# Optimization experiments

Measured on AMD Instinct MI355X. Metric: run time of the kernel, lower is better.

## Reference

```python
import jax, jax.numpy as jnp
import numpy as np

N = 50000
C = 128
E = 800000
STEPS = 3


def setup_inputs() -> dict:
    key = jax.random.key(0)
    ks = jax.random.split(key, 8)
    x = jax.random.normal(ks[0], (N, C), dtype=jnp.float32)
    edge_index = jax.random.randint(ks[1], (2, E), 0, N, dtype=jnp.int64)
    s = 1.0 / np.sqrt(C)
    W_lin = jax.random.uniform(ks[2], (C, C), jnp.float32, -s, s)   # nn.Linear(C, C, bias=False)
    W_ih = jax.random.uniform(ks[3], (3 * C, C), jnp.float32, -s, s)  # GRUCell weight_ih
    W_hh = jax.random.uniform(ks[4], (3 * C, C), jnp.float32, -s, s)  # GRUCell weight_hh
    b_ih = jax.random.uniform(ks[5], (3 * C,), jnp.float32, -s, s)
    b_hh = jax.random.uniform(ks[6], (3 * C,), jnp.float32, -s, s)
    return {"x": x, "edge_index": edge_index, "W_lin": W_lin,
            "W_ih": W_ih, "W_hh": W_hh, "b_ih": b_ih, "b_hh": b_hh}


def _gru_cell(inp, h, W_ih, W_hh, b_ih, b_hh):
    # torch.nn.GRUCell math
    gi = inp @ W_ih.T + b_ih   # [N, 3C]
    gh = h @ W_hh.T + b_hh     # [N, 3C]
    i_r, i_z, i_n = jnp.split(gi, 3, axis=-1)
    h_r, h_z, h_n = jnp.split(gh, 3, axis=-1)
    r = jax.nn.sigmoid(i_r + h_r)
    z = jax.nn.sigmoid(i_z + h_z)
    n = jnp.tanh(i_n + r * h_n)
    return (1.0 - z) * n + z * h


def reference(x, edge_index, W_lin, W_ih, W_hh, b_ih, b_hh):
    src = edge_index[0]
    dst = edge_index[1]
    state = x
    for _ in range(STEPS):
        m = state @ W_lin.T                       # [N, C] dense transform
        msgs = jnp.take(m, src, axis=0)           # [E, C] gather
        propagated = jax.ops.segment_sum(msgs, dst, num_segments=N)  # scatter-add
        state = _gru_cell(propagated, state, W_ih, W_hh, b_ih, b_hh)
    return state
```

## Files before the change

### kernel.cpp

```cpp
#include <hip/hip_runtime.h>

#define NN 50000
#define CC 128
#define EE 800000
#define NT 1563
#define NBLK 196

typedef short bf16x8 __attribute__((ext_vector_type(8)));
typedef float f32x4 __attribute__((ext_vector_type(4)));

__device__ __forceinline__ float bf2f(unsigned int u16) {
  union { unsigned int u; float f; } x; x.u = u16 << 16; return x.f;
}
__device__ __forceinline__ unsigned short f2bf(float f) {
  union { float f; unsigned int u; } x; x.f = f;
  unsigned int u = x.u;
  unsigned int r = (u + 0x7fffu + ((u >> 16) & 1u)) >> 16;
  return (unsigned short)r;
}

__global__ void cast_f2b_k(const float* __restrict__ in, unsigned short* __restrict__ out, int n4) {
  int i = blockIdx.x * blockDim.x + threadIdx.x;
  int stride = gridDim.x * blockDim.x;
  for (; i < n4; i += stride) {
    float4 v = ((const float4*)in)[i];
    ushort4 o;
    o.x = f2bf(v.x); o.y = f2bf(v.y); o.z = f2bf(v.z); o.w = f2bf(v.w);
    ((ushort4*)out)[i] = o;
  }
}

__global__ __launch_bounds__(256) void wcomp_k(const float* __restrict__ Wih,
                                               const float* __restrict__ Wlin,
                                               unsigned short* __restrict__ Wcb) {
  int gid = blockIdx.x * 256 + threadIdx.x;
  int i = gid >> 7, j = gid & 127;
  float acc = 0.f;
  #pragma unroll 8
  for (int k = 0; k < 128; ++k)
    acc += Wih[i * 128 + k] * Wlin[k * 128 + j];
  Wcb[i * 128 + j] = f2bf(acc);
}

__global__ void zero_k(int* __restrict__ p, int n) {
  int i = blockIdx.x * blockDim.x + threadIdx.x;
  if (i < n) p[i] = 0;
}

__global__ void hist_k(const int* __restrict__ dst, int* __restrict__ cnt, int n) {
  int i = blockIdx.x * blockDim.x + threadIdx.x;
  if (i < n) atomicAdd(&cnt[dst[i]], 1);
}

__global__ __launch_bounds__(256) void scan1_k(const int* __restrict__ cnt,
                                               int* __restrict__ rowptr,
                                               int* __restrict__ bsum, int N) {
  __shared__ int wtot[4];
  int tid = threadIdx.x, lane = tid & 63, w = tid >> 6;
  int i = blockIdx.x * 256 + tid;
  int v = (i < N) ? cnt[i] : 0;
  int x = v;
  #pragma unroll
  for (int off = 1; off < 64; off <<= 1) {
    int t = __shfl_up(x, off, 64);
    if (lane >= off) x += t;
  }
  if (lane == 63) wtot[w] = x;
  __syncthreads();
  int woff = 0;
  for (int j = 0; j < w; ++j) woff += wtot[j];
  int excl = x - v + woff;
  if (i < N) rowptr[i] = excl;
  if (tid == 255) bsum[blockIdx.x] = excl + v;
}

__global__ __launch_bounds__(256) void scan2_k(int* __restrict__ bsum, int* __restrict__ rowptr, int NB) {
  __shared__ int wtot[4];
  int tid = threadIdx.x, lane = tid & 63, w = tid >> 6;
  int v = (tid < NB) ? bsum[tid] : 0;
  int x = v;
  #pragma unroll
  for (int off = 1; off < 64; off <<= 1) {
    int t = __shfl_up(x, off, 64);
    if (lane >= off) x += t;
  }
  if (lane == 63) wtot[w] = x;
  __syncthreads();
  int woff = 0;
  for (int j = 0; j < w; ++j) woff += wtot[j];
  int excl = x - v + woff;
  if (tid < NB) bsum[tid] = excl;
  if (tid == 255) rowptr[NN] = excl + v;
}

__global__ void scan3_k(int* __restrict__ rowptr, const int* __restrict__ bsum,
                        int* __restrict__ cursor, int N) {
  int i = blockIdx.x * 256 + threadIdx.x;
  if (i < N) {
    int r = rowptr[i] + bsum[i >> 8];
    rowptr[i] = r;
    cursor[i] = r;
  }
}

__global__ void fill_k(const int* __restrict__ src, const int* __restrict__ dst,
                       int* __restrict__ cursor, int* __restrict__ colx, int n) {
  int i = blockIdx.x * blockDim.x + threadIdx.x;
  if (i < n) {
    int pos = atomicAdd(&cursor[dst[i]], 1);
    colx[pos] = src[i];
  }
}

__global__ __launch_bounds__(256) void agg2_k(const unsigned short* __restrict__ M,
                                              const int* __restrict__ rowptr,
                                              const int* __restrict__ colx,
                                              unsigned short* __restrict__ P, int N) {
  int wid = (blockIdx.x * 256 + threadIdx.x) >> 6;
  int lane = threadIdx.x & 63;
  if (wid >= N) return;
  int beg = rowptr[wid], end = rowptr[wid + 1];
  int half = lane >> 5, li = lane & 31;
  float a0 = 0.f, a1 = 0.f, a2 = 0.f, a3 = 0.f;
  int n = end - beg;
  int i = 0;
  for (; i + 8 <= n; i += 8) {
    int e = beg + i + half;
    int s0 = colx[e], s1 = colx[e + 2], s2 = colx[e + 4], s3 = colx[e + 6];
    uint2 v0 = *(const uint2*)(M + s0 * CC + li * 4);
    uint2 v1 = *(const uint2*)(M + s1 * CC + li * 4);
    uint2 v2 = *(const uint2*)(M + s2 * CC + li * 4);
    uint2 v3 = *(const uint2*)(M + s3 * CC + li * 4);
    a0 += bf2f(v0.x & 0xffffu); a1 += bf2f(v0.x >> 16); a2 += bf2f(v0.y & 0xffffu); a3 += bf2f(v0.y >> 16);
    a0 += bf2f(v1.x & 0xffffu); a1 += bf2f(v1.x >> 16); a2 += bf2f(v1.y & 0xffffu); a3 += bf2f(v1.y >> 16);
    a0 += bf2f(v2.x & 0xffffu); a1 += bf2f(v2.x >> 16); a2 += bf2f(v2.y & 0xffffu); a3 += bf2f(v2.y >> 16);
    a0 += bf2f(v3.x & 0xffffu); a1 += bf2f(v3.x >> 16); a2 += bf2f(v3.y & 0xffffu); a3 += bf2f(v3.y >> 16);
  }
  for (; i + 2 <= n; i += 2) {
    int e = beg + i + half;
    int s = colx[e];
    uint2 v = *(const uint2*)(M + s * CC + li * 4);
    a0 += bf2f(v.x & 0xffffu); a1 += bf2f(v.x >> 16); a2 += bf2f(v.y & 0xffffu); a3 += bf2f(v.y >> 16);
  }
  if (i < n && half == 0) {
    int s = colx[beg + i];
    uint2 v = *(const uint2*)(M + s * CC + li * 4);
    a0 += bf2f(v.x & 0xffffu); a1 += bf2f(v.x >> 16); a2 += bf2f(v.y & 0xffffu); a3 += bf2f(v.y >> 16);
  }
  a0 += __shfl_xor(a0, 32, 64);
  a1 += __shfl_xor(a1, 32, 64);
  a2 += __shfl_xor(a2, 32, 64);
  a3 += __shfl_xor(a3, 32, 64);
  if (half == 0) {
    uint2 o;
    o.x = (unsigned int)f2bf(a0) | ((unsigned int)f2bf(a1) << 16);
    o.y = (unsigned int)f2bf(a2) | ((unsigned int)f2bf(a3) << 16);
    *(uint2*)(P + wid * CC + li * 4) = o;
  }
}

__global__ __launch_bounds__(256, 2) void gru3_k(const unsigned short* __restrict__ Pb,
                                                 const unsigned short* __restrict__ Sb_in,
                                                 unsigned short* __restrict__ Sb_out,
                                                 const float* __restrict__ h_in,
                                                 float* __restrict__ h_out,
                                                 const unsigned short* __restrict__ Wcb,
                                                 const unsigned short* __restrict__ Whhb,
                                                 const float* __restrict__ bih,
                                                 const float* __restrict__ bhh) {
  __shared__ unsigned short sA[2][2][32][128];
  const int tid = threadIdx.x;
  const int half = blockIdx.x & 1;
  const int group = blockIdx.x >> 1;
  const int lane = tid & 63, w = tid >> 6;
  const int l15 = lane & 15, l4 = lane >> 4;

  const int c_loc = w * 16 + l15;
  const int cg = half * 64 + c_loc;

  bf16x8 Breg[6][4];
  #pragma unroll
  for (int pi = 0; pi < 6; ++pi) {
    const unsigned short* Wm = (pi < 3) ? Wcb : Whhb;
    int p = (pi < 3) ? pi : pi - 3;
    const unsigned short* base = Wm + (p * 128 + cg) * 128 + l4 * 8;
    #pragma unroll
    for (int ks = 0; ks < 4; ++ks)
      Breg[pi][ks] = *(const bf16x8*)(base + ks * 32);
  }

  const float bir = bih[cg], biz = bih[cg + 128], bin_ = bih[cg + 256];
  const float bhr = bhh[cg], bhz = bhh[cg + 128], bhn = bhh[cg + 256];

  auto loadA = [&](int t, uint4* r) {
    int rowbase = t * 32;
    #pragma unroll
    for (int k = 0; k < 4; ++k) {
      int idx = k * 256 + tid;
      int mat = idx >> 9, j = idx & 511, row = j >> 4, ch = j & 15;
      int grow = rowbase + row;
      const unsigned short* srcp = mat ? Sb_in : Pb;
      r[k] = (grow < NN) ? *(const uint4*)(srcp + grow * 128 + ch * 8) : make_uint4(0, 0, 0, 0);
    }
  };
  auto writeA = [&](int buf, const uint4* r) {
    #pragma unroll
    for (int k = 0; k < 4; ++k) {
      int idx = k * 256 + tid;
      int mat = idx >> 9, j = idx & 511, row = j >> 4, ch = j & 15;
      *(uint4*)&sA[buf][mat][row][((ch ^ (row & 15)) * 8)] = r[k];
    }
  };

  uint4 pre[4];
  int t0 = group;
  loadA(t0, pre);
  writeA(0, pre);
  int cur = 0;
  for (int t = t0; t < NT; t += 256) {
    __syncthreads();
    int tn = t + 256;
    uint4 nxt[4];
    if (tn < NT) loadA(tn, nxt);

    f32x4 acc[6][2] = {};
    #pragma unroll
    for (int ks = 0; ks < 4; ++ks) {
      bf16x8 a[2][2];
      #pragma unroll
      for (int mat = 0; mat < 2; ++mat)
        #pragma unroll
        for (int rt = 0; rt < 2; ++rt) {
          int row = rt * 16 + l15;
          a[mat][rt] = *(const bf16x8*)&sA[cur][mat][row][(((ks * 4 + l4) ^ l15) * 8)];
        }
      #pragma unroll
      for (int pi = 0; pi < 6; ++pi) {
        int am = (pi < 3) ? 0 : 1;
        acc[pi][0] = __builtin_amdgcn_mfma_f32_16x16x32_bf16(a[am][0], Breg[pi][ks], acc[pi][0], 0, 0, 0);
        acc[pi][1] = __builtin_amdgcn_mfma_f32_16x16x32_bf16(a[am][1], Breg[pi][ks], acc[pi][1], 0, 0, 0);
      }
    }

    int rowbase = t * 32;
    #pragma unroll
    for (int rt = 0; rt < 2; ++rt)
      #pragma unroll
      for (int i = 0; i < 4; ++i) {
        int row = rowbase + rt * 16 + l4 * 4 + i;
        if (row < NN) {
          float gir = acc[0][rt][i] + bir;
          float giz = acc[1][rt][i] + biz;
          float gin = acc[2][rt][i] + bin_;
          float ghr = acc[3][rt][i] + bhr;
          float ghz = acc[4][rt][i] + bhz;
          float ghn = acc[5][rt][i] + bhn;
          float r = 1.f / (1.f + __expf(-(gir + ghr)));
          float z = 1.f / (1.f + __expf(-(giz + ghz)));
          float n = tanhf(gin + r * ghn);
          float h = h_in[row * 128 + cg];
          float o = (1.f - z) * n + z * h;
          h_out[row * 128 + cg] = o;
          Sb_out[row * 128 + cg] = f2bf(o);
        }
      }
    if (tn < NT) writeA(cur ^ 1, nxt);
    cur ^= 1;
  }
}

extern "C" void kernel_launch(void* const* d_in, const int* in_sizes, int n_in,
                              void* d_out, int out_size, void* d_ws, size_t ws_size,
                              hipStream_t stream) {
  const float* x    = (const float*)d_in[0];
  const int*   ei   = (const int*)d_in[1];
  const float* Wlin = (const float*)d_in[2];
  const float* Wih  = (const float*)d_in[3];
  const float* Whh  = (const float*)d_in[4];
  const float* bih  = (const float*)d_in[5];
  const float* bhh  = (const float*)d_in[6];
  float* out = (float*)d_out;

  char* ws = (char*)d_ws;
  size_t off = 0;
  auto alloc = [&](size_t bytes) -> void* {
    void* p = ws + off;
    off += (bytes + 255) & ~(size_t)255;
    return p;
  };
  unsigned short* SbA  = (unsigned short*)alloc((size_t)NN * CC * 2);
  unsigned short* SbB  = (unsigned short*)alloc((size_t)NN * CC * 2);
  unsigned short* Prb  = (unsigned short*)alloc((size_t)NN * CC * 2);
  float*          Sf   = (float*)alloc((size_t)NN * CC * 4);
  unsigned short* Wcb  = (unsigned short*)alloc((size_t)3 * CC * CC * 2);
  unsigned short* Whhb = (unsigned short*)alloc((size_t)3 * CC * CC * 2);
  int* rowptr = (int*)alloc((size_t)(NN + 1) * 4);
  int* cursor = (int*)alloc((size_t)NN * 4);
  int* colx   = (int*)alloc((size_t)EE * 4);
  int* bsum   = (int*)alloc(256 * 4);

  const int* srcI = ei;
  const int* dstI = ei + EE;

  cast_f2b_k<<<1024, 256, 0, stream>>>(x, SbA, NN * CC / 4);
  cast_f2b_k<<<48, 256, 0, stream>>>(Whh, Whhb, 3 * CC * CC / 4);
  wcomp_k<<<192, 256, 0, stream>>>(Wih, Wlin, Wcb);

  zero_k<<<NBLK, 256, 0, stream>>>(cursor, NN);
  hist_k<<<(EE + 255) / 256, 256, 0, stream>>>(dstI, cursor, EE);
  scan1_k<<<NBLK, 256, 0, stream>>>(cursor, rowptr, bsum, NN);
  scan2_k<<<1, 256, 0, stream>>>(bsum, rowptr, NBLK);
  scan3_k<<<NBLK, 256, 0, stream>>>(rowptr, bsum, cursor, NN);
  fill_k<<<(EE + 255) / 256, 256, 0, stream>>>(srcI, dstI, cursor, colx, EE);

  const int aggBlocks = (NN + 3) / 4;

  agg2_k<<<aggBlocks, 256, 0, stream>>>(SbA, rowptr, colx, Prb, NN);
  gru3_k<<<512, 256, 0, stream>>>(Prb, SbA, SbB, x, Sf, Wcb, Whhb, bih, bhh);
  agg2_k<<<aggBlocks, 256, 0, stream>>>(SbB, rowptr, colx, Prb, NN);
  gru3_k<<<512, 256, 0, stream>>>(Prb, SbB, SbA, Sf, Sf, Wcb, Whhb, bih, bhh);
  agg2_k<<<aggBlocks, 256, 0, stream>>>(SbA, rowptr, colx, Prb, NN);
  gru3_k<<<512, 256, 0, stream>>>(Prb, SbA, SbB, Sf, out, Wcb, Whhb, bih, bhh);
}
```

Baseline: 395.7 us.

## Merge weight prep kernels, vectorize CSR build, use fast GRU activations

Fuses the Whh cast and the Wih·Wlin composition into one launch. Vectorizes the histogram and CSR fill kernels to load four edge indices per thread with int4. Replaces the sigmoid and tanh in the GRU epilogue with fast-division, exp-based forms. The fill kernel now writes colx with atomic exchanges, and the fast tanh may lose some accuracy or overflow at extreme inputs.

```diff
diff --git a/kernel.cpp b/kernel.cpp
--- a/kernel.cpp
+++ b/kernel.cpp
@@ -17,6 +17,12 @@
   unsigned int u = x.u;
   unsigned int r = (u + 0x7fffu + ((u >> 16) & 1u)) >> 16;
   return (unsigned short)r;
+}
+__device__ __forceinline__ float fsigmoid(float x) {
+  return __fdividef(1.f, 1.f + __expf(-x));
+}
+__device__ __forceinline__ float ftanh(float x) {
+  return 1.f - __fdividef(2.f, 1.f + __expf(2.f * x));
 }
 
 __global__ void cast_f2b_k(const float* __restrict__ in, unsigned short* __restrict__ out, int n4) {
@@ -30,16 +36,26 @@
   }
 }
 
-__global__ __launch_bounds__(256) void wcomp_k(const float* __restrict__ Wih,
+__global__ __launch_bounds__(256) void wprep_k(const float* __restrict__ Wih,
                                                const float* __restrict__ Wlin,
-                                               unsigned short* __restrict__ Wcb) {
-  int gid = blockIdx.x * 256 + threadIdx.x;
-  int i = gid >> 7, j = gid & 127;
-  float acc = 0.f;
-  #pragma unroll 8
-  for (int k = 0; k < 128; ++k)
-    acc += Wih[i * 128 + k] * Wlin[k * 128 + j];
-  Wcb[i * 128 + j] = f2bf(acc);
+                                               const float* __restrict__ Whh,
+                                               unsigned short* __restrict__ Wcb,
+                                               unsigned short* __restrict__ Whhb) {
+  if (blockIdx.x < 192) {
+    int gid = blockIdx.x * 256 + threadIdx.x;
+    int i = gid >> 7, j = gid & 127;
+    float acc = 0.f;
+    #pragma unroll 8
+    for (int k = 0; k < 128; ++k)
+      acc += Wih[i * 128 + k] * Wlin[k * 128 + j];
+    Wcb[i * 128 + j] = f2bf(acc);
+  } else {
+    int i = (blockIdx.x - 192) * 256 + threadIdx.x;
+    float4 v = ((const float4*)Whh)[i];
+    ushort4 o;
+    o.x = f2bf(v.x); o.y = f2bf(v.y); o.z = f2bf(v.z); o.w = f2bf(v.w);
+    ((ushort4*)Whhb)[i] = o;
+  }
 }
 
 __global__ void zero_k(int* __restrict__ p, int n) {
@@ -47,9 +63,15 @@
   if (i < n) p[i] = 0;
 }
 
-__global__ void hist_k(const int* __restrict__ dst, int* __restrict__ cnt, int n) {
+__global__ void hist_k(const int* __restrict__ dst, int* __restrict__ cnt, int n4) {
   int i = blockIdx.x * blockDim.x + threadIdx.x;
-  if (i < n) atomicAdd(&cnt[dst[i]], 1);
+  if (i < n4) {
+    int4 d = ((const int4*)dst)[i];
+    atomicAdd(&cnt[d.x], 1);
+    atomicAdd(&cnt[d.y], 1);
+    atomicAdd(&cnt[d.z], 1);
+    atomicAdd(&cnt[d.w], 1);
+  }
 }
 
 __global__ __launch_bounds__(256) void scan1_k(const int* __restrict__ cnt,
@@ -104,11 +126,19 @@
 }
 
 __global__ void fill_k(const int* __restrict__ src, const int* __restrict__ dst,
-                       int* __restrict__ cursor, int* __restrict__ colx, int n) {
+                       int* __restrict__ cursor, int* __restrict__ colx, int n4) {
   int i = blockIdx.x * blockDim.x + threadIdx.x;
-  if (i < n) {
-    int pos = atomicAdd(&cursor[dst[i]], 1);
-    colx[pos] = src[i];
+  if (i < n4) {
+    int4 s = ((const int4*)src)[i];
+    int4 d = ((const int4*)dst)[i];
+    int p0 = atomicAdd(&cursor[d.x], 1);
+    int p1 = atomicAdd(&cursor[d.y], 1);
+    int p2 = atomicAdd(&cursor[d.z], 1);
+    int p3 = atomicAdd(&cursor[d.w], 1);
+    atomicExch(&colx[p0], s.x);
+    atomicExch(&colx[p1], s.y);
+    atomicExch(&colx[p2], s.z);
+    atomicExch(&colx[p3], s.w);
   }
 }
 
@@ -255,11 +285,11 @@
           float ghr = acc[3][rt][i] + bhr;
           float ghz = acc[4][rt][i] + bhz;
           float ghn = acc[5][rt][i] + bhn;
-          float r = 1.f / (1.f + __expf(-(gir + ghr)));
-          float z = 1.f / (1.f + __expf(-(giz + ghz)));
-          float n = tanhf(gin + r * ghn);
+          float r = fsigmoid(gir + ghr);
+          float z = fsigmoid(giz + ghz);
+          float n = ftanh(gin + r * ghn);
           float h = h_in[row * 128 + cg];
-          float o = (1.f - z) * n + z * h;
+          float o = n + z * (h - n);
           h_out[row * 128 + cg] = o;
           Sb_out[row * 128 + cg] = f2bf(o);
         }
@@ -303,15 +333,14 @@
   const int* dstI = ei + EE;
 
   cast_f2b_k<<<1024, 256, 0, stream>>>(x, SbA, NN * CC / 4);
-  cast_f2b_k<<<48, 256, 0, stream>>>(Whh, Whhb, 3 * CC * CC / 4);
-  wcomp_k<<<192, 256, 0, stream>>>(Wih, Wlin, Wcb);
+  wprep_k<<<240, 256, 0, stream>>>(Wih, Wlin, Whh, Wcb, Whhb);
 
   zero_k<<<NBLK, 256, 0, stream>>>(cursor, NN);
-  hist_k<<<(EE + 255) / 256, 256, 0, stream>>>(dstI, cursor, EE);
+  hist_k<<<(EE / 4 + 255) / 256, 256, 0, stream>>>(dstI, cursor, EE / 4);
   scan1_k<<<NBLK, 256, 0, stream>>>(cursor, rowptr, bsum, NN);
   scan2_k<<<1, 256, 0, stream>>>(bsum, rowptr, NBLK);
   scan3_k<<<NBLK, 256, 0, stream>>>(rowptr, bsum, cursor, NN);
-  fill_k<<<(EE + 255) / 256, 256, 0, stream>>>(srcI, dstI, cursor, colx, EE);
+  fill_k<<<(EE / 4 + 255) / 256, 256, 0, stream>>>(srcI, dstI, cursor, colx, EE / 4);
 
   const int aggBlocks = (NN + 3) / 4;
 
```

Result: no change. 401.9 us (+1.6%).
